# Kernel optimization log

Measured on AMD Instinct MI355X. Metric: run time of the kernel, lower is better.

Reference implementation:

```python
import jax, jax.numpy as jnp
import numpy as np
from functools import partial

H = 51  # hidden size hard-coded in the module


def _lstm_cell(x, h, c, W_ih, b_ih, W_hh, b_hh):
    # PyTorch LSTMCell gate order: i, f, g, o stacked along dim 0 of W (4H rows)
    gates = x @ W_ih.T + b_ih + h @ W_hh.T + b_hh  # [B, 4H]
    i, f, g, o = jnp.split(gates, 4, axis=-1)
    i = jax.nn.sigmoid(i)
    f = jax.nn.sigmoid(f)
    g = jnp.tanh(g)
    o = jax.nn.sigmoid(o)
    c_new = f * c + i * g
    h_new = o * jnp.tanh(c_new)
    return h_new, c_new


def setup_inputs() -> dict:
    key = jax.random.key(0)
    ks = jax.random.split(key, 11)
    B, T = 2048, 512
    bound = 1.0 / np.sqrt(H)  # torch LSTMCell/Linear default init: U(-1/sqrt(H), 1/sqrt(H))
    u = lambda k, shape: jax.random.uniform(k, shape, jnp.float32, -bound, bound)
    return {
        "x": jax.random.normal(ks[0], (B, T), dtype=jnp.float32),
        "future": 0,
        "W_ih1": u(ks[1], (4 * H, 1)),
        "b_ih1": u(ks[2], (4 * H,)),
        "W_hh1": u(ks[3], (4 * H, H)),
        "b_hh1": u(ks[4], (4 * H,)),
        "W_ih2": u(ks[5], (4 * H, H)),
        "b_ih2": u(ks[6], (4 * H,)),
        "W_hh2": u(ks[7], (4 * H, H)),
        "b_hh2": u(ks[8], (4 * H,)),
        "fc_w": u(ks[9], (1, H)),
        "fc_b": u(ks[10], (1,)),
    }


def reference(x, future, W_ih1, b_ih1, W_hh1, b_hh1,
              W_ih2, b_ih2, W_hh2, b_hh2, fc_w, fc_b):
    B = x.shape[0]
    z = jnp.zeros((B, H), dtype=x.dtype)

    def cell_stack(x_t, carry):
        h1, c1, h2, c2 = carry
        h1, c1 = _lstm_cell(x_t, h1, c1, W_ih1, b_ih1, W_hh1, b_hh1)
        h2, c2 = _lstm_cell(h1, h2, c2, W_ih2, b_ih2, W_hh2, b_hh2)
        out = h2 @ fc_w.T + fc_b  # [B, 1]
        return (h1, c1, h2, c2), out

    def step(carry, x_t):
        return cell_stack(x_t, carry)

    xs = jnp.swapaxes(x, 0, 1)[:, :, None]  # [T, B, 1]
    carry, outs = jax.lax.scan(step, (z, z, z, z), xs)  # outs: [T, B, 1]
    outputs = jnp.swapaxes(outs[:, :, 0], 0, 1)  # [B, T]

    if future > 0:
        last = outs[-1]  # [B, 1]

        def fstep(c, _):
            inner, out = c
            inner, out = cell_stack(out, inner)
            return (inner, out), out

        _, fouts = jax.lax.scan(fstep, (carry, last), None, length=future)
        outputs = jnp.concatenate([outputs, jnp.swapaxes(fouts[:, :, 0], 0, 1)], axis=1)

    return outputs
```

## Files before the change

### kernel.cpp

```cpp
#include <hip/hip_runtime.h>

#define HID   51
#define T_LEN 512
#define BT    8
#define NTH   832

#define X_OFF   0
#define OUT_OFF 4128
#define H_OFF   8256

typedef _Float16 h8 __attribute__((ext_vector_type(8)));
typedef float    f4 __attribute__((ext_vector_type(4)));

__device__ __forceinline__ float fast_rcp(float x) { return __builtin_amdgcn_rcpf(x); }
__device__ __forceinline__ float sigm(float x) { return fast_rcp(1.0f + __expf(-x)); }
__device__ __forceinline__ float tanh_f(float x) {
    x = fminf(15.0f, fmaxf(-15.0f, x));
    float e = __expf(2.0f * x);
    return (e - 1.0f) * fast_rcp(e + 1.0f);
}
__device__ __forceinline__ float tanh_nc(float x) {
    float e = __expf(2.0f * x);
    return (e - 1.0f) * fast_rcp(e + 1.0f);
}

__device__ __forceinline__ float dpp_ror8(float v) {
    int t = __builtin_amdgcn_update_dpp(0, __float_as_int(v), 0x128, 0xf, 0xf, true);
    return __int_as_float(t);
}

__device__ __forceinline__ h8 cvt_frag1(const float* p) {
    float4 a = *(const float4*)p;
    float4 b = *(const float4*)(p + 4);
    h8 h;
    h[0] = (_Float16)a.x; h[1] = (_Float16)a.y; h[2] = (_Float16)a.z; h[3] = (_Float16)a.w;
    h[4] = (_Float16)b.x; h[5] = (_Float16)b.y; h[6] = (_Float16)b.z; h[7] = (_Float16)b.w;
    return h;
}

__device__ __forceinline__ float gate_update(const float G[4], float& c) {
    float iv = sigm(G[0]), fv = sigm(G[1]), gv = tanh_nc(G[2]), ov = sigm(G[3]);
    c = fv * c + iv * gv;
    return ov * tanh_f(c);
}

#define MFMA16(A, B, C) __builtin_amdgcn_mfma_f32_16x16x32_f16((A), (B), (C), 0, 0, 0)

__global__ __launch_bounds__(NTH)
void lstm_seq_kernel(const float* __restrict__ x,
                     const float* __restrict__ W_ih1, const float* __restrict__ b_ih1,
                     const float* __restrict__ W_hh1, const float* __restrict__ b_hh1,
                     const float* __restrict__ W_ih2, const float* __restrict__ b_ih2,
                     const float* __restrict__ W_hh2, const float* __restrict__ b_hh2,
                     const float* __restrict__ fc_w,  const float* __restrict__ fc_b,
                     float* __restrict__ out)
{
    __shared__ __align__(16) float sb[13312];

    const int tid   = threadIdx.x;
    const int b0    = blockIdx.x * BT;
    const int w     = tid >> 6;
    const int lane  = tid & 63;
    const int row16 = lane & 15;
    const int q4    = lane >> 4;
    const int col   = row16;

    h8 a1f[2];
    h8 a2if[2];
    h8 a2hf[2];

    for (int i = tid; i < 208 * 64; i += NTH) {
        int rp = i >> 6, k = i & 63;
        int j = rp >> 2, g = rp & 3;
        float v = 0.0f;
        if (j < HID) {
            if (k < HID)       v = W_hh1[(g * HID + j) * HID + k];
            else if (k == HID) v = W_ih1[g * HID + j];
        }
        sb[i] = v;
    }
    __syncthreads();
    #pragma unroll
    for (int kt = 0; kt < 2; ++kt)
        a1f[kt] = cvt_frag1(sb + (w * 16 + row16) * 64 + kt * 32 + q4 * 8);
    __syncthreads();

    for (int i = tid; i < 208 * 64; i += NTH) {
        int rp = i >> 6, k = i & 63;
        int j = rp >> 2, g = rp & 3;
        sb[i] = (j < HID && k < HID) ? W_ih2[(g * HID + j) * HID + k] : 0.0f;
    }
    __syncthreads();
    #pragma unroll
    for (int kt = 0; kt < 2; ++kt)
        a2if[kt] = cvt_frag1(sb + (w * 16 + row16) * 64 + kt * 32 + q4 * 8);
    __syncthreads();

    for (int i = tid; i < 208 * 64; i += NTH) {
        int rp = i >> 6, k = i & 63;
        int j = rp >> 2, g = rp & 3;
        float v = 0.0f;
        if (k < HID) {
            if (j < HID)        v = W_hh2[(g * HID + j) * HID + k];
            else if (rp == 204) v = fc_w[k];
        }
        sb[i] = v;
    }
    __syncthreads();
    #pragma unroll
    for (int kt = 0; kt < 2; ++kt)
        a2hf[kt] = cvt_frag1(sb + (w * 16 + row16) * 64 + kt * 32 + q4 * 8);
    __syncthreads();

    const int jq = 4 * w + q4;
    f4 bi1, bi2;
    #pragma unroll
    for (int g = 0; g < 4; ++g) {
        bi1[g] = (jq < HID) ? (b_ih1[g * HID + jq] + b_hh1[g * HID + jq]) : 0.f;
        bi2[g] = (jq < HID) ? (b_ih2[g * HID + jq] + b_hh2[g * HID + jq]) : 0.f;
    }
    const bool lay1 = (col < 8);
    const int  bsel = col & 7;
    const bool val  = (jq < HID);
    const int  cpos = lay1 ? bsel : (8 + bsel);
    const int  offh = H_OFF * 2
                    + (jq >> 5) * 512 + ((((jq & 31) >> 3) << 4) + cpos) * 8 + (jq & 7);
    const bool xw = (jq == HID) && lay1;

    float* xl   = sb + X_OFF;
    float* outl = sb + OUT_OFF;
    for (int i = tid; i < BT * 516; i += NTH) {
        int b = i / 516, t = i - 516 * b;
        xl[i] = (t < T_LEN) ? x[(size_t)(b0 + b) * T_LEN + t] : 0.0f;
    }
    for (int i = tid; i < 1024; i += NTH) sb[H_OFF + i] = 0.0f;

    float c = 0.f;
    const float fcb = fc_b[0];
    const bool outlane = (w == 12) && (q4 == 3) && (col >= 8);
    const float* xq  = xl + bsel * 516;
    const float* rA0 = sb + H_OFF + lane * 4;
    _Float16* hwp = (_Float16*)sb + offh;
    __syncthreads();

    if (lay1) {
        if (val) {
            float xv = xq[0];
            float G[4];
            #pragma unroll
            for (int g = 0; g < 4; ++g)
                G[g] = bi1[g] + W_ih1[g * HID + jq] * xv;
            float hv = gate_update(G, c);
            hwp[0] = (_Float16)hv;
        } else if (xw) {
            hwp[0] = (_Float16)xq[1];
        }
    }
    __syncthreads();

    auto body = [&](int i, int p) {
        const float* rA = rA0 + p * 512;
        h8 bb0 = *(const h8*)(rA);       h8 bb1 = *(const h8*)(rA + 256);

        if (xw) hwp[(p ^ 1) * 1024] = (_Float16)xq[i + 2];

        f4 s = bi1;
        s = MFMA16(a1f[0], bb0, s);
        s = MFMA16(a1f[1], bb1, s);
        f4 u = {0.f, 0.f, 0.f, 0.f};
        u = MFMA16(a2if[0], bb0, u);
        u = MFMA16(a2if[1], bb1, u);
        f4 v = bi2;
        v = MFMA16(a2hf[0], bb0, v);
        v = MFMA16(a2hf[1], bb1, v);

        float fcv = v[0];
        float G[4];
        #pragma unroll
        for (int g = 0; g < 4; ++g) {
            float ug = dpp_ror8(u[g]) + v[g];
            G[g] = lay1 ? s[g] : ug;
        }
        float hv = gate_update(G, c);
        if (val) hwp[(p ^ 1) * 1024] = (_Float16)hv;
        if (outlane && i >= 1) outl[(col - 8) * 516 + (i - 1)] = fcb + fcv;
        __syncthreads();
    };
    for (int i = 0; i < T_LEN; i += 2) {
        body(i, 0);
        body(i + 1, 1);
    }
    body(T_LEN, 0);

    for (int i = tid; i < BT * T_LEN; i += NTH) {
        int b = i >> 9, tt = i & (T_LEN - 1);
        out[(size_t)(b0 + b) * T_LEN + tt] = outl[b * 516 + tt];
    }
}

extern "C" void kernel_launch(void* const* d_in, const int* in_sizes, int n_in,
                              void* d_out, int out_size, void* d_ws, size_t ws_size,
                              hipStream_t stream) {
    const float* x      = (const float*)d_in[0];
    const float* W_ih1  = (const float*)d_in[2];
    const float* b_ih1v = (const float*)d_in[3];
    const float* W_hh1  = (const float*)d_in[4];
    const float* b_hh1v = (const float*)d_in[5];
    const float* W_ih2  = (const float*)d_in[6];
    const float* b_ih2v = (const float*)d_in[7];
    const float* W_hh2  = (const float*)d_in[8];
    const float* b_hh2v = (const float*)d_in[9];
    const float* fc_w   = (const float*)d_in[10];
    const float* fc_b   = (const float*)d_in[11];
    float* out = (float*)d_out;

    dim3 grid(2048 / BT);
    dim3 block(NTH);
    lstm_seq_kernel<<<grid, block, 0, stream>>>(x, W_ih1, b_ih1v, W_hh1, b_hh1v,
                                                W_ih2, b_ih2v, W_hh2, b_hh2v,
                                                fc_w, fc_b, out);
}
```

Before: 378.0 us.

## Halve batch tile per block and give each wave two M-tiles

Reduces the batch tile from 8 to 4 rows and the block from 13 to 8 waves. Each wave now computes two 16-row gate tiles (doubling its MFMA count per step), and the 4 batch columns are duplicated across the 16-wide B operand so every lane quadrant selects its own tile's result. Launch bounds request 4 blocks per CU. The aim is more blocks resident per CU and fewer waves at each per-step barrier, so independent blocks can hide each other's latency. The cost is twice as many blocks, doubled MFMA work per useful row, and more registers per wave.

```diff
diff --git a/kernel.cpp b/kernel.cpp
--- a/kernel.cpp
+++ b/kernel.cpp
@@ -2,12 +2,12 @@
 
 #define HID   51
 #define T_LEN 512
-#define BT    8
-#define NTH   832
+#define BT    4
+#define NTH   512
 
 #define X_OFF   0
-#define OUT_OFF 4128
-#define H_OFF   8256
+#define OUT_OFF 2064
+#define H_OFF   4128
 
 typedef _Float16 h8 __attribute__((ext_vector_type(8)));
 typedef float    f4 __attribute__((ext_vector_type(4)));
@@ -46,7 +46,7 @@
 
 #define MFMA16(A, B, C) __builtin_amdgcn_mfma_f32_16x16x32_f16((A), (B), (C), 0, 0, 0)
 
-__global__ __launch_bounds__(NTH)
+__global__ __launch_bounds__(NTH, 4)
 void lstm_seq_kernel(const float* __restrict__ x,
                      const float* __restrict__ W_ih1, const float* __restrict__ b_ih1,
                      const float* __restrict__ W_hh1, const float* __restrict__ b_hh1,
@@ -64,10 +64,14 @@
     const int row16 = lane & 15;
     const int q4    = lane >> 4;
     const int col   = row16;
-
-    h8 a1f[2];
-    h8 a2if[2];
-    h8 a2hf[2];
+    const int cq    = col >> 2;
+
+    const int mt0 = w;
+    const int mt1 = (w < 5) ? 8 + w : 12;
+
+    h8 a1f[2][2];
+    h8 a2if[2][2];
+    h8 a2hf[2][2];
 
     for (int i = tid; i < 208 * 64; i += NTH) {
         int rp = i >> 6, k = i & 63;
@@ -81,8 +85,12 @@
     }
     __syncthreads();
     #pragma unroll
-    for (int kt = 0; kt < 2; ++kt)
-        a1f[kt] = cvt_frag1(sb + (w * 16 + row16) * 64 + kt * 32 + q4 * 8);
+    for (int s = 0; s < 2; ++s) {
+        int mt = s ? mt1 : mt0;
+        #pragma unroll
+        for (int kt = 0; kt < 2; ++kt)
+            a1f[s][kt] = cvt_frag1(sb + (mt * 16 + row16) * 64 + kt * 32 + q4 * 8);
+    }
     __syncthreads();
 
     for (int i = tid; i < 208 * 64; i += NTH) {
@@ -92,8 +100,12 @@
     }
     __syncthreads();
     #pragma unroll
-    for (int kt = 0; kt < 2; ++kt)
-        a2if[kt] = cvt_frag1(sb + (w * 16 + row16) * 64 + kt * 32 + q4 * 8);
+    for (int s = 0; s < 2; ++s) {
+        int mt = s ? mt1 : mt0;
+        #pragma unroll
+        for (int kt = 0; kt < 2; ++kt)
+            a2if[s][kt] = cvt_frag1(sb + (mt * 16 + row16) * 64 + kt * 32 + q4 * 8);
+    }
     __syncthreads();
 
     for (int i = tid; i < 208 * 64; i += NTH) {
@@ -108,24 +120,33 @@
     }
     __syncthreads();
     #pragma unroll
-    for (int kt = 0; kt < 2; ++kt)
-        a2hf[kt] = cvt_frag1(sb + (w * 16 + row16) * 64 + kt * 32 + q4 * 8);
-    __syncthreads();
-
-    const int jq = 4 * w + q4;
-    f4 bi1, bi2;
+    for (int s = 0; s < 2; ++s) {
+        int mt = s ? mt1 : mt0;
+        #pragma unroll
+        for (int kt = 0; kt < 2; ++kt)
+            a2hf[s][kt] = cvt_frag1(sb + (mt * 16 + row16) * 64 + kt * 32 + q4 * 8);
+    }
+    __syncthreads();
+
+    const int jq0 = 4 * mt0 + q4;
+    const int jq1 = 4 * mt1 + q4;
+    f4 bi1s0, bi1s1, bi2s0, bi2s1;
     #pragma unroll
     for (int g = 0; g < 4; ++g) {
-        bi1[g] = (jq < HID) ? (b_ih1[g * HID + jq] + b_hh1[g * HID + jq]) : 0.f;
-        bi2[g] = (jq < HID) ? (b_ih2[g * HID + jq] + b_hh2[g * HID + jq]) : 0.f;
-    }
-    const bool lay1 = (col < 8);
-    const int  bsel = col & 7;
-    const bool val  = (jq < HID);
+        bi1s0[g] = (jq0 < HID) ? (b_ih1[g * HID + jq0] + b_hh1[g * HID + jq0]) : 0.f;
+        bi1s1[g] = (jq1 < HID) ? (b_ih1[g * HID + jq1] + b_hh1[g * HID + jq1]) : 0.f;
+        bi2s0[g] = (jq0 < HID) ? (b_ih2[g * HID + jq0] + b_hh2[g * HID + jq0]) : 0.f;
+        bi2s1[g] = (jq1 < HID) ? (b_ih2[g * HID + jq1] + b_hh2[g * HID + jq1]) : 0.f;
+    }
+
+    const int  jsel = (cq & 1) ? jq1 : jq0;
+    const bool lay1 = (cq < 2);
+    const int  bsel = col & 3;
+    const bool val  = (jsel < HID);
     const int  cpos = lay1 ? bsel : (8 + bsel);
     const int  offh = H_OFF * 2
-                    + (jq >> 5) * 512 + ((((jq & 31) >> 3) << 4) + cpos) * 8 + (jq & 7);
-    const bool xw = (jq == HID) && lay1;
+                    + (jsel >> 5) * 512 + ((((jsel & 31) >> 3) << 4) + cpos) * 8 + (jsel & 7);
+    const bool xw = (jsel == HID) && lay1;
 
     float* xl   = sb + X_OFF;
     float* outl = sb + OUT_OFF;
@@ -137,7 +158,7 @@
 
     float c = 0.f;
     const float fcb = fc_b[0];
-    const bool outlane = (w == 12) && (q4 == 3) && (col >= 8);
+    const bool outlane = (w == 5) && (q4 == 3) && (cq == 3);
     const float* xq  = xl + bsel * 516;
     const float* rA0 = sb + H_OFF + lane * 4;
     _Float16* hwp = (_Float16*)sb + offh;
@@ -146,14 +167,17 @@
     if (lay1) {
         if (val) {
             float xv = xq[0];
+            f4 bb = (cq == 0) ? bi1s0 : bi1s1;
             float G[4];
             #pragma unroll
             for (int g = 0; g < 4; ++g)
-                G[g] = bi1[g] + W_ih1[g * HID + jq] * xv;
+                G[g] = bb[g] + W_ih1[g * HID + jsel] * xv;
             float hv = gate_update(G, c);
-            hwp[0] = (_Float16)hv;
+            _Float16 h16 = (_Float16)hv;
+            hwp[0] = h16; hwp[32] = h16;
         } else if (xw) {
-            hwp[0] = (_Float16)xq[1];
+            _Float16 x16 = (_Float16)xq[1];
+            hwp[0] = x16; hwp[32] = x16;
         }
     }
     __syncthreads();
@@ -162,28 +186,37 @@
         const float* rA = rA0 + p * 512;
         h8 bb0 = *(const h8*)(rA);       h8 bb1 = *(const h8*)(rA + 256);
 
-        if (xw) hwp[(p ^ 1) * 1024] = (_Float16)xq[i + 2];
-
-        f4 s = bi1;
-        s = MFMA16(a1f[0], bb0, s);
-        s = MFMA16(a1f[1], bb1, s);
-        f4 u = {0.f, 0.f, 0.f, 0.f};
-        u = MFMA16(a2if[0], bb0, u);
-        u = MFMA16(a2if[1], bb1, u);
-        f4 v = bi2;
-        v = MFMA16(a2hf[0], bb0, v);
-        v = MFMA16(a2hf[1], bb1, v);
-
-        float fcv = v[0];
+        if (xw) {
+            _Float16 x16 = (_Float16)xq[i + 2];
+            hwp[(p ^ 1) * 1024] = x16; hwp[(p ^ 1) * 1024 + 32] = x16;
+        }
+
+        f4 s0 = bi1s0, s1 = bi1s1;
+        s0 = MFMA16(a1f[0][0], bb0, s0); s1 = MFMA16(a1f[1][0], bb0, s1);
+        s0 = MFMA16(a1f[0][1], bb1, s0); s1 = MFMA16(a1f[1][1], bb1, s1);
+        f4 u0 = {0.f,0.f,0.f,0.f}, u1 = u0;
+        u0 = MFMA16(a2if[0][0], bb0, u0); u1 = MFMA16(a2if[1][0], bb0, u1);
+        u0 = MFMA16(a2if[0][1], bb1, u0); u1 = MFMA16(a2if[1][1], bb1, u1);
+        f4 v0 = bi2s0, v1 = bi2s1;
+        v0 = MFMA16(a2hf[0][0], bb0, v0); v1 = MFMA16(a2hf[1][0], bb0, v1);
+        v0 = MFMA16(a2hf[0][1], bb1, v0); v1 = MFMA16(a2hf[1][1], bb1, v1);
+
+        float fcv = v1[0];
         float G[4];
         #pragma unroll
         for (int g = 0; g < 4; ++g) {
-            float ug = dpp_ror8(u[g]) + v[g];
-            G[g] = lay1 ? s[g] : ug;
+            float t2 = dpp_ror8(u0[g]) + v0[g];
+            float t3 = dpp_ror8(u1[g]) + v1[g];
+            float t01 = (cq == 0) ? s0[g] : s1[g];
+            float t23 = (cq == 2) ? t2 : t3;
+            G[g] = lay1 ? t01 : t23;
         }
         float hv = gate_update(G, c);
-        if (val) hwp[(p ^ 1) * 1024] = (_Float16)hv;
-        if (outlane && i >= 1) outl[(col - 8) * 516 + (i - 1)] = fcb + fcv;
+        _Float16 h16 = (_Float16)hv;
+        if (val) {
+            hwp[(p ^ 1) * 1024] = h16; hwp[(p ^ 1) * 1024 + 32] = h16;
+        }
+        if (outlane && i >= 1) outl[bsel * 516 + (i - 1)] = fcb + fcv;
         __syncthreads();
     };
     for (int i = 0; i < T_LEN; i += 2) {
```

New measurement: 494.5 us. 30.8% more time.
